# Kernel optimization log

Measured on AMD Instinct MI355X. Metric: run time of the kernel, lower is better.

Reference implementation:

```python
import jax, jax.numpy as jnp
from jax import lax
import numpy as np

DN = ('NCDHW', 'OIDHW', 'NCDHW')
ACTIVE_THRESH = 1


def setup_inputs() -> dict:
    key = jax.random.key(0)
    ks = jax.random.split(key, 10)
    B, D = 4, 64
    chans = [3, 64, 128, 256, 512]
    inp = {
        'x': jax.random.normal(ks[0], (B, 3, D, D, D), jnp.float32),
        'mask': jax.random.randint(ks[1], (B, D, D, D), 0, 20, jnp.int32),
    }
    for i in range(4):
        cin, cout = chans[i], chans[i + 1]
        fan_in = cin * 27
        scale = 1.0 / np.sqrt(fan_in)
        inp[f'w{i+1}'] = jax.random.normal(ks[2 + 2 * i], (cout, cin, 3, 3, 3), jnp.float32) * scale
        inp[f'b{i+1}'] = jax.random.normal(ks[3 + 2 * i], (cout,), jnp.float32) * scale
    return inp


def _sparse_block(x, m, w, b, stride):
    # SparseConv3d(k=3, pad=1) + SparseReLU: output active where 3^3 footprint hits an active input;
    # bias + relu applied only at active sites, inactive sites stay exactly 0 (spconv .dense() semantics).
    s = (stride,) * 3
    pad = [(1, 1)] * 3
    y = lax.conv_general_dilated(x, w, s, pad, dimension_numbers=DN)
    ones = jnp.ones((1, 1, 3, 3, 3), x.dtype)
    m_out = lax.conv_general_dilated(m[:, None].astype(x.dtype), ones, s, pad, dimension_numbers=DN) > 0
    y = jnp.where(m_out, jax.nn.relu(y + b[None, :, None, None, None]), jnp.zeros((), x.dtype))
    return y, m_out[:, 0]


def reference(x, mask, w1, b1, w2, b2, w3, b3, w4, b4):
    m = mask < ACTIVE_THRESH                       # [B,D,H,W] active voxels
    h = x * m[:, None].astype(x.dtype)             # zero inactive input features
    h, m = _sparse_block(h, m, w1, b1, 1)          # [B,64,64,64,64]
    h, m = _sparse_block(h, m, w2, b2, 2)          # [B,128,32,32,32]
    h, m = _sparse_block(h, m, w3, b3, 2)          # [B,256,16,16,16]
    h, m = _sparse_block(h, m, w4, b4, 2)          # [B,512,8,8,8]
    pooled = jnp.max(h, axis=(2, 3, 4))            # dense() + amax over D,H,W -> [B,512]
    return jax.nn.leaky_relu(pooled, negative_slope=0.2)
```

## Files before the change

### kernel.cpp

```cpp
#include <hip/hip_runtime.h>

typedef _Float16 f16;
typedef _Float16 half4 __attribute__((ext_vector_type(4)));
typedef _Float16 half8 __attribute__((ext_vector_type(8)));
typedef float f32x4 __attribute__((ext_vector_type(4)));

#define BATCH 4

__device__ __forceinline__ void gload16(const void* g, void* l) {
  __builtin_amdgcn_global_load_lds((const __attribute__((address_space(1))) unsigned int*)g,
                                   (__attribute__((address_space(3))) unsigned int*)l, 16, 0, 0);
}

template<int DP, int ROWB>
__global__ __launch_bounds__(256) void zborder_k(char* __restrict__ buf) {
  int v = blockIdx.x * 256 + threadIdx.x;
  int b = blockIdx.y;
  if (v >= DP * DP * DP) return;
  int w = v % DP; int t = v / DP; int h = t % DP; int d = t / DP;
  bool border = (w == 0) | (w == DP - 1) | (h == 0) | (h == DP - 1) | (d == 0) | (d == DP - 1);
  if (!border) return;
  char* p = buf + ((size_t)b * DP * DP * DP + v) * ROWB;
  #pragma unroll
  for (int i = 0; i < ROWB; i += 8)
    *reinterpret_cast<unsigned long long*>(p + i) = 0ull;
}

__global__ __launch_bounds__(256) void wprep_k(const float* __restrict__ w,
                                               f16* __restrict__ w27, int COUT, int CIN) {
  int idx = blockIdx.x * 256 + threadIdx.x;
  int total = COUT * CIN * 27;
  if (idx >= total) return;
  int k = idx % 27;
  int t = idx / 27;
  int ci = t % CIN;
  int co = t / CIN;
  w27[((size_t)k * COUT + co) * CIN + ci] = (f16)w[idx];
}

__global__ __launch_bounds__(256) void wprep1_k(const float* __restrict__ w,
                                                f16* __restrict__ wf) {
  int idx = blockIdx.x * 256 + threadIdx.x;
  if (idx >= 64 * 128) return;
  int q = idx & 127, co = idx >> 7;
  int k = q >> 2, ci = q & 3;
  float v = (ci < 3 && k < 27) ? w[(co * 3 + ci) * 27 + k] : 0.f;
  wf[idx] = (f16)v;
}

__global__ __launch_bounds__(256) void xmask_k(const float* __restrict__ x,
                                               const int* __restrict__ mask,
                                               f16* __restrict__ xcp) {
  const int D3 = 262144, PD = 66, PD3 = PD * PD * PD;
  int v = blockIdx.x * 256 + threadIdx.x;
  int b = blockIdx.y;
  bool act = mask[(size_t)b * D3 + v] < 1;
  const float* xb = x + (size_t)b * 3 * D3 + v;
  half4 o;
  o[0] = act ? (f16)xb[0] : (f16)0.f;
  o[1] = act ? (f16)xb[D3] : (f16)0.f;
  o[2] = act ? (f16)xb[2 * D3] : (f16)0.f;
  o[3] = (f16)0.f;
  int ow = v & 63, oh = (v >> 6) & 63, od = v >> 12;
  size_t pv = ((size_t)(od + 1) * PD + oh + 1) * PD + ow + 1;
  *reinterpret_cast<half4*>(xcp + ((size_t)b * PD3 + pv) * 4) = o;
}

__global__ __launch_bounds__(256) void dil_w_k(const int* __restrict__ mask,
                                               unsigned char* __restrict__ aw) {
  const int D3 = 262144;
  int t = blockIdx.x * 256 + threadIdx.x;
  int b = t >> 16;
  int v = (t & 65535) * 4;
  int w0 = v & 63;
  const int* mb = mask + (size_t)b * D3;
  int a[6];
  a[0] = (w0 > 0) ? (mb[v - 1] < 1) : 0;
  #pragma unroll
  for (int i = 0; i < 4; i++) a[i + 1] = mb[v + i] < 1;
  a[5] = (w0 < 60) ? (mb[v + 4] < 1) : 0;
  unsigned int o = 0;
  #pragma unroll
  for (int i = 0; i < 4; i++)
    o |= ((unsigned)(a[i] | a[i + 1] | a[i + 2])) << (8 * i);
  *reinterpret_cast<unsigned int*>(aw + (size_t)b * D3 + v) = o;
}

template<int STRIDE, int DIMSHIFT>
__global__ __launch_bounds__(256) void dil_hd_k(const unsigned char* __restrict__ ai,
                                                unsigned char* __restrict__ ao) {
  const int D3 = 262144;
  int t = blockIdx.x * 256 + threadIdx.x;
  int b = t >> 16;
  int v = (t & 65535) * 4;
  int c = (v >> DIMSHIFT) & 63;
  const unsigned char* ib = ai + (size_t)b * D3;
  unsigned int m = *reinterpret_cast<const unsigned int*>(ib + v);
  if (c > 0)  m |= *reinterpret_cast<const unsigned int*>(ib + v - STRIDE);
  if (c < 63) m |= *reinterpret_cast<const unsigned int*>(ib + v + STRIDE);
  *reinterpret_cast<unsigned int*>(ao + (size_t)b * D3 + v) = m;
}

template<int DIN, int DOUT>
__global__ __launch_bounds__(256) void dilate_s2_k(const unsigned char* __restrict__ mi,
                                                   unsigned char* __restrict__ mo) {
  const int Do3 = DOUT * DOUT * DOUT;
  int v = blockIdx.x * 256 + threadIdx.x;
  if (v >= Do3) return;
  int b = blockIdx.y;
  int ow = v % DOUT, t = v / DOUT, oh = t % DOUT, od = t / DOUT;
  const unsigned char* ib = mi + (size_t)b * DIN * DIN * DIN;
  int act = 0;
  for (int kd = 0; kd < 3; kd++) { int id = od * 2 - 1 + kd; if ((unsigned)id >= (unsigned)DIN) continue;
    for (int kh = 0; kh < 3; kh++) { int ih = oh * 2 - 1 + kh; if ((unsigned)ih >= (unsigned)DIN) continue;
      for (int kw = 0; kw < 3; kw++) { int iw = ow * 2 - 1 + kw; if ((unsigned)iw >= (unsigned)DIN) continue;
        act |= ib[((size_t)id * DIN + ih) * DIN + iw];
      } } }
  mo[(size_t)b * Do3 + v] = (unsigned char)(act ? 1 : 0);
}

template<int BM>
__global__ __launch_bounds__(256) void conv1_mfma_k(const f16* __restrict__ xcp,
                                                    const f16* __restrict__ w1f,
                                                    const float* __restrict__ bias,
                                                    const unsigned char* __restrict__ mo,
                                                    f16* __restrict__ out ) {
  const int D3 = 262144, COUT = 64, PD = 66, PD3 = PD * PD * PD;
  constexpr int K = 128, LD = K + 8;
  constexpr int WM = 2, WN = 2;
  constexpr int MF = BM / (16 * WM), NF = 64 / (16 * WN);
  __shared__ __align__(16) f16 As[BM][LD];
  __shared__ __align__(16) f16 Bs[64][LD];

  const int tid = threadIdx.x, lane = tid & 63, wave = tid >> 6;
  const int wm = wave >> 1, wn = wave & 1;
  const int v0 = blockIdx.x * BM;
  const int b = blockIdx.y;
  const f16* xb = xcp + (size_t)b * PD3 * 4;

  for (int c = tid; c < 64 * (K / 8); c += 256) {
    int row = c >> 4, cc = c & 15;
    *reinterpret_cast<half8*>(&Bs[row][cc * 8]) =
        *reinterpret_cast<const half8*>(w1f + row * K + cc * 8);
  }
  {
    const int row = tid & (BM - 1);
    const int v = v0 + row;
    const int ow = v & 63, oh = (v >> 6) & 63, od = v >> 12;
    const int base = (od * PD + oh) * PD + ow;
    for (int e = tid; e < 32 * BM; e += 256) {
      int kslot = e / BM;
      half4 val = {};
      if (kslot < 27) {
        int kd = kslot / 9, r2 = kslot - kd * 9, kh = r2 / 3, kw = r2 - kh * 3;
        val = *reinterpret_cast<const half4*>(xb + (size_t)(base + (kd * PD + kh) * PD + kw) * 4);
      }
      *reinterpret_cast<half4*>(&As[row][kslot * 4]) = val;
    }
  }
  __syncthreads();

  f32x4 acc[MF][NF] = {};
  const int chanoff = (lane >> 4) << 3;
  const int arow = wm * MF * 16 + (lane & 15);
  const int brow = wn * NF * 16 + (lane & 15);
  #pragma unroll
  for (int q0 = 0; q0 < K; q0 += 32) {
    half8 a[MF], bb[NF];
    #pragma unroll
    for (int mf = 0; mf < MF; mf++)
      a[mf] = *reinterpret_cast<const half8*>(&As[arow + mf * 16][q0 + chanoff]);
    #pragma unroll
    for (int nf = 0; nf < NF; nf++)
      bb[nf] = *reinterpret_cast<const half8*>(&Bs[brow + nf * 16][q0 + chanoff]);
    #pragma unroll
    for (int mf = 0; mf < MF; mf++)
      #pragma unroll
      for (int nf = 0; nf < NF; nf++)
        acc[mf][nf] = __builtin_amdgcn_mfma_f32_16x16x32_f16(a[mf], bb[nf], acc[mf][nf], 0, 0, 0);
  }

  const unsigned char* mb = mo + (size_t)b * D3;
  f16* ob = out + (size_t)b * PD3 * COUT;
  const int ll = lane & 15, lh = lane >> 4;
  float bv[NF];
  #pragma unroll
  for (int nf = 0; nf < NF; nf++) bv[nf] = bias[wn * NF * 16 + nf * 16 + ll];
  #pragma unroll
  for (int mf = 0; mf < MF; mf++) {
    #pragma unroll
    for (int r = 0; r < 4; r++) {
      int v = v0 + wm * MF * 16 + mf * 16 + (lh << 2) + r;
      bool act = mb[v] != 0;
      int ow = v & 63, oh = (v >> 6) & 63, od = v >> 12;
      size_t pv = ((size_t)(od + 1) * PD + oh + 1) * PD + ow + 1;
      #pragma unroll
      for (int nf = 0; nf < NF; nf++) {
        int co = wn * NF * 16 + nf * 16 + ll;
        float val = acc[mf][nf][r] + bv[nf];
        val = act ? (val > 0.f ? val : 0.f) : 0.f;
        ob[pv * COUT + co] = (f16)val;
      }
    }
  }
}

template<int CINS, int CINF, int COUT, int DIN, int DOUT, int BM, int BN,
         int WM, int WN, int SWZ, int OP>
__global__ __launch_bounds__(WM * WN * 64) void conv_mfma2_k(const f16* __restrict__ in,
                                                             const f16* __restrict__ w27,
                                                             const float* __restrict__ bias,
                                                             const unsigned char* __restrict__ mo,
                                                             f16* __restrict__ out) {
  constexpr int PD = DIN + 2, PDo = DOUT + 2;
  constexpr int NW = WM * WN;
  constexpr int MF = BM / (16 * WM), NF = BN / (16 * WN);
  constexpr int ROWB = CINS * 2;
  constexpr int ROWBF = CINF * 2;
  constexpr int CHUNKS = ROWB / 16;
  constexpr int RPI = 64 / CHUNKS;
  constexpr int A_IW = BM / RPI / NW;
  constexpr int B_IW = BN / RPI / NW;
  constexpr int CIH = CINF / CINS;
  constexpr int NSTEP = 27 * CIH;
  constexpr int D3o = DOUT * DOUT * DOUT;
  constexpr int LOGD = (DOUT == 32) ? 5 : ((DOUT == 16) ? 4 : 3);

  __shared__ __align__(16) char As[2][BM * ROWB];
  __shared__ __align__(16) char Bs[2][BN * ROWB];

  const int tid = threadIdx.x, lane = tid & 63, wave = tid >> 6;
  const int wm = wave / WN, wn = wave % WN;
  int bx = blockIdx.x;
  if (SWZ) {
    int cpx = gridDim.x >> 3;
    bx = (bx & 7) * cpx + (bx >> 3);
  }
  const int v0 = bx * BM, co0 = blockIdx.y * BN, b = blockIdx.z;
  const char* ib = (const char*)(in + (size_t)b * PD * PD * PD * CINF);

  const int lrow = lane / CHUNKS;
  const int lchunk = lane % CHUNKS;
  const char* a_src[A_IW];
  #pragma unroll
  for (int i = 0; i < A_IW; i++) {
    int r = (wave * A_IW + i) * RPI + lrow;
    int v = v0 + r;
    int ow = v & (DOUT - 1), oh = (v >> LOGD) & (DOUT - 1), od = v >> (2 * LOGD);
    size_t flat = ((size_t)(2 * od) * PD + 2 * oh) * PD + 2 * ow;
    a_src[i] = ib + flat * ROWBF + (lchunk ^ (r & 7)) * 16;
  }
  const char* b_src[B_IW];
  #pragma unroll
  for (int i = 0; i < B_IW; i++) {
    int r = (wave * B_IW + i) * RPI + lrow;
    b_src[i] = (const char*)w27 + (size_t)(co0 + r) * ROWBF + (lchunk ^ (r & 7)) * 16;
  }

  auto stage = [&](int buf, int s) {
    int k = (CIH == 2) ? (s >> 1) : s;
    int h = (CIH == 2) ? (s & 1) : 0;
    int kd = k / 9, r2 = k - kd * 9, kh = r2 / 3, kw = r2 - kh * 3;
    int koff = ((kd * PD + kh) * PD + kw) * ROWBF + h * ROWB;
    #pragma unroll
    for (int i = 0; i < A_IW; i++)
      gload16(a_src[i] + koff, &As[buf][(wave * A_IW + i) * 1024]);
    size_t wko = (size_t)k * COUT * ROWBF + h * ROWB;
    #pragma unroll
    for (int i = 0; i < B_IW; i++)
      gload16(b_src[i] + wko, &Bs[buf][(wave * B_IW + i) * 1024]);
  };

  f32x4 acc[MF][NF] = {};
  const int ll = lane & 15, lh = lane >> 4;
  const int ra0 = wm * MF * 16 + ll;
  const int rb0 = wn * NF * 16 + ll;
  const int rswa = ra0 & 7;
  const int rswb = rb0 & 7;

  stage(0, 0);
  __syncthreads();
  int cur = 0;
  for (int s = 0; s < NSTEP; s++) {
    if (s < NSTEP - 1) stage(cur ^ 1, s + 1);
    #pragma unroll
    for (int ci0 = 0; ci0 < CINS; ci0 += 32) {
      const int q = (ci0 >> 3) + lh;
      half8 a[MF], bb[NF];
      #pragma unroll
      for (int mf = 0; mf < MF; mf++)
        a[mf] = *reinterpret_cast<const half8*>(
            &As[cur][(ra0 + mf * 16) * ROWB + ((q ^ rswa) * 16)]);
      #pragma unroll
      for (int nf = 0; nf < NF; nf++)
        bb[nf] = *reinterpret_cast<const half8*>(
            &Bs[cur][(rb0 + nf * 16) * ROWB + ((q ^ rswb) * 16)]);
      #pragma unroll
      for (int mf = 0; mf < MF; mf++)
        #pragma unroll
        for (int nf = 0; nf < NF; nf++)
          acc[mf][nf] = __builtin_amdgcn_mfma_f32_16x16x32_f16(a[mf], bb[nf], acc[mf][nf], 0, 0, 0);
    }
    __syncthreads();
    cur ^= 1;
  }

  const unsigned char* mb = mo + (size_t)b * D3o;
  f16* ob = out + (size_t)b * (OP ? PDo * PDo * PDo : D3o) * COUT;
  float bv[NF];
  #pragma unroll
  for (int nf = 0; nf < NF; nf++) bv[nf] = bias[co0 + wn * NF * 16 + nf * 16 + ll];
  #pragma unroll
  for (int mf = 0; mf < MF; mf++) {
    #pragma unroll
    for (int r = 0; r < 4; r++) {
      int v = v0 + wm * MF * 16 + mf * 16 + (lh << 2) + r;
      bool act = mb[v] != 0;
      int ow = v & (DOUT - 1), oh = (v >> LOGD) & (DOUT - 1), od = v >> (2 * LOGD);
      size_t pv = OP ? (((size_t)(od + 1) * PDo + oh + 1) * PDo + ow + 1) : (size_t)v;
      #pragma unroll
      for (int nf = 0; nf < NF; nf++) {
        int co = co0 + wn * NF * 16 + nf * 16 + ll;
        float val = acc[mf][nf][r] + bv[nf];
        val = act ? (val > 0.f ? val : 0.f) : 0.f;
        ob[pv * COUT + co] = (f16)val;
      }
    }
  }
}

__global__ __launch_bounds__(256) void pool_k(const f16* __restrict__ h4,
                                              float* __restrict__ outp) {
  __shared__ float red[4][64];
  int b = blockIdx.y;
  int cl = threadIdx.x & 63;
  int co = blockIdx.x * 64 + cl;
  int vg = threadIdx.x >> 6;
  const f16* p = h4 + (size_t)b * 512 * 512;
  float m = 0.f;
  for (int v = vg * 128; v < vg * 128 + 128; v++) m = fmaxf(m, (float)p[(size_t)v * 512 + co]);
  red[vg][cl] = m;
  __syncthreads();
  if (threadIdx.x < 64) {
    m = fmaxf(fmaxf(red[0][threadIdx.x], red[1][threadIdx.x]),
              fmaxf(red[2][threadIdx.x], red[3][threadIdx.x]));
    float r = (m >= 0.f) ? m : 0.2f * m;
    outp[b * 512 + blockIdx.x * 64 + threadIdx.x] = r;
  }
}

extern "C" void kernel_launch(void* const* d_in, const int* in_sizes, int n_in,
                              void* d_out, int out_size, void* d_ws, size_t ws_size,
                              hipStream_t stream) {
  const float* x    = (const float*)d_in[0];
  const int*   mask = (const int*)d_in[1];
  const float* w1 = (const float*)d_in[2];
  const float* b1 = (const float*)d_in[3];
  const float* w2 = (const float*)d_in[4];
  const float* b2 = (const float*)d_in[5];
  const float* w3 = (const float*)d_in[6];
  const float* b3 = (const float*)d_in[7];
  const float* w4 = (const float*)d_in[8];
  const float* b4 = (const float*)d_in[9];
  float* outp = (float*)d_out;

  const size_t PD1 = 66 * 66 * 66;
  const size_t PD2 = 34 * 34 * 34;
  const size_t PD3s = 18 * 18 * 18;

  char* ws = (char*)d_ws;
  size_t off = 0;
  auto alloc = [&](size_t bytes) -> char* {
    char* p = ws + off;
    off = (off + bytes + 255) & ~(size_t)255;
    return p;
  };
  f16* wf1 = (f16*)alloc((size_t)64 * 128 * 2);
  f16* wf2 = (f16*)alloc((size_t)27 * 128 * 64 * 2);
  f16* wf3 = (f16*)alloc((size_t)27 * 256 * 128 * 2);
  f16* wf4 = (f16*)alloc((size_t)27 * 512 * 256 * 2);
  unsigned char* aw = (unsigned char*)alloc((size_t)BATCH * 262144);
  unsigned char* ah = (unsigned char*)alloc((size_t)BATCH * 262144);
  unsigned char* m1 = (unsigned char*)alloc((size_t)BATCH * 262144);
  unsigned char* m2 = (unsigned char*)alloc((size_t)BATCH * 32768);
  unsigned char* m3 = (unsigned char*)alloc((size_t)BATCH * 4096);
  unsigned char* m4 = (unsigned char*)alloc((size_t)BATCH * 512);
  f16* h1p = (f16*)alloc((size_t)BATCH * PD1 * 64 * 2);
  f16* h2p = (f16*)alloc((size_t)BATCH * PD2 * 128 * 2);
  f16* h3p = (f16*)alloc((size_t)BATCH * PD3s * 256 * 2);
  f16* h4  = (f16*)alloc((size_t)BATCH * 512 * 512 * 2);
  f16* xcp = h3p;
  if (off > ws_size) return;

  wprep1_k<<<dim3((64 * 128 + 255) / 256), 256, 0, stream>>>(w1, wf1);
  wprep_k<<<dim3((128 * 64 * 27 + 255) / 256), 256, 0, stream>>>(w2, wf2, 128, 64);
  wprep_k<<<dim3((256 * 128 * 27 + 255) / 256), 256, 0, stream>>>(w3, wf3, 256, 128);
  wprep_k<<<dim3((512 * 256 * 27 + 255) / 256), 256, 0, stream>>>(w4, wf4, 512, 256);

  dil_w_k<<<dim3(BATCH * 65536 / 256), 256, 0, stream>>>(mask, aw);
  dil_hd_k<64, 6><<<dim3(BATCH * 65536 / 256), 256, 0, stream>>>(aw, ah);
  dil_hd_k<4096, 12><<<dim3(BATCH * 65536 / 256), 256, 0, stream>>>(ah, m1);
  dilate_s2_k<64, 32><<<dim3(128, BATCH), 256, 0, stream>>>(m1, m2);
  dilate_s2_k<32, 16><<<dim3(16, BATCH), 256, 0, stream>>>(m2, m3);
  dilate_s2_k<16, 8><<<dim3(2, BATCH), 256, 0, stream>>>(m3, m4);

  xmask_k<<<dim3(1024, BATCH), 256, 0, stream>>>(x, mask, xcp);
  zborder_k<66, 8><<<dim3((287496 + 255) / 256, BATCH), 256, 0, stream>>>((char*)xcp);
  zborder_k<66, 128><<<dim3((287496 + 255) / 256, BATCH), 256, 0, stream>>>((char*)h1p);
  zborder_k<34, 256><<<dim3((39304 + 255) / 256, BATCH), 256, 0, stream>>>((char*)h2p);

  conv1_mfma_k<128><<<dim3(262144 / 128, BATCH), 256, 0, stream>>>(xcp, wf1, b1, m1, h1p);

  zborder_k<18, 512><<<dim3((5832 + 255) / 256, BATCH), 256, 0, stream>>>((char*)h3p);

  conv_mfma2_k<64, 64, 128, 64, 32, 64, 128, 2, 2, 1, 1>
      <<<dim3(512, 1, BATCH), 256, 0, stream>>>(h1p, wf2, b2, m2, h2p);
  conv_mfma2_k<64, 128, 256, 32, 16, 64, 64, 2, 2, 0, 1>
      <<<dim3(64, 4, BATCH), 256, 0, stream>>>(h2p, wf3, b3, m3, h3p);
  conv_mfma2_k<128, 256, 512, 16, 8, 32, 64, 1, 2, 0, 0>
      <<<dim3(16, 8, BATCH), 128, 0, stream>>>(h3p, wf4, b4, m4, h4);

  pool_k<<<dim3(8, BATCH), 256, 0, stream>>>(h4, outp);
}
```

Measured before the change: 351.8 us.

## Load conv weights directly into registers, enlarge tiles, merge batch in conv4

The implicit-GEMM conv kernel stops staging weight tiles in shared memory. Each lane now loads its B fragments straight from global memory into registers, double-buffered across step pairs, while only the activation tile still goes through LDS. Tile sizes grow (BM 128 for conv2, BN 128 for conv3, 64x128 with 4 waves for conv4), and conv4 folds the batch into the M dimension to get larger tiles and fewer blocks. This cuts LDS traffic and footprint but adds register pressure and uncoalesced global weight reads that rely on cache reuse.

```diff
diff --git a/kernel.cpp b/kernel.cpp
--- a/kernel.cpp
+++ b/kernel.cpp
@@ -206,8 +206,8 @@
 }
 
 template<int CINS, int CINF, int COUT, int DIN, int DOUT, int BM, int BN,
-         int WM, int WN, int SWZ, int OP>
-__global__ __launch_bounds__(WM * WN * 64) void conv_mfma2_k(const f16* __restrict__ in,
+         int WM, int WN, int SWZ, int OP, int BMERGE>
+__global__ __launch_bounds__(WM * WN * 64) void conv_mfmaR_k(const f16* __restrict__ in,
                                                              const f16* __restrict__ w27,
                                                              const float* __restrict__ bias,
                                                              const unsigned char* __restrict__ mo,
@@ -220,14 +220,14 @@
   constexpr int CHUNKS = ROWB / 16;
   constexpr int RPI = 64 / CHUNKS;
   constexpr int A_IW = BM / RPI / NW;
-  constexpr int B_IW = BN / RPI / NW;
   constexpr int CIH = CINF / CINS;
   constexpr int NSTEP = 27 * CIH;
+  constexpr int CI0S = CINS / 32;
+  constexpr int NBF = NF * CI0S;
   constexpr int D3o = DOUT * DOUT * DOUT;
   constexpr int LOGD = (DOUT == 32) ? 5 : ((DOUT == 16) ? 4 : 3);
 
   __shared__ __align__(16) char As[2][BM * ROWB];
-  __shared__ __align__(16) char Bs[2][BN * ROWB];
 
   const int tid = threadIdx.x, lane = tid & 63, wave = tid >> 6;
   const int wm = wave / WN, wn = wave % WN;
@@ -236,8 +236,8 @@
     int cpx = gridDim.x >> 3;
     bx = (bx & 7) * cpx + (bx >> 3);
   }
-  const int v0 = bx * BM, co0 = blockIdx.y * BN, b = blockIdx.z;
-  const char* ib = (const char*)(in + (size_t)b * PD * PD * PD * CINF);
+  const int v0 = bx * BM, co0 = blockIdx.y * BN;
+  const int bz = BMERGE ? 0 : blockIdx.z;
 
   const int lrow = lane / CHUNKS;
   const int lchunk = lane % CHUNKS;
@@ -246,18 +246,21 @@
   for (int i = 0; i < A_IW; i++) {
     int r = (wave * A_IW + i) * RPI + lrow;
     int v = v0 + r;
-    int ow = v & (DOUT - 1), oh = (v >> LOGD) & (DOUT - 1), od = v >> (2 * LOGD);
-    size_t flat = ((size_t)(2 * od) * PD + 2 * oh) * PD + 2 * ow;
-    a_src[i] = ib + flat * ROWBF + (lchunk ^ (r & 7)) * 16;
-  }
-  const char* b_src[B_IW];
-  #pragma unroll
-  for (int i = 0; i < B_IW; i++) {
-    int r = (wave * B_IW + i) * RPI + lrow;
-    b_src[i] = (const char*)w27 + (size_t)(co0 + r) * ROWBF + (lchunk ^ (r & 7)) * 16;
-  }
-
-  auto stage = [&](int buf, int s) {
+    int vb = BMERGE ? (v >> (3 * LOGD)) : bz;
+    int vv = BMERGE ? (v & (D3o - 1)) : v;
+    int ow = vv & (DOUT - 1), oh = (vv >> LOGD) & (DOUT - 1), od = vv >> (2 * LOGD);
+    size_t flat = (size_t)vb * PD * PD * PD + ((size_t)(2 * od) * PD + 2 * oh) * PD + 2 * ow;
+    a_src[i] = (const char*)in + flat * ROWBF + (lchunk ^ (r & 7)) * 16;
+  }
+  const int ll = lane & 15, lh = lane >> 4;
+  const char* b_src[NF];
+  #pragma unroll
+  for (int nf = 0; nf < NF; nf++) {
+    int row = co0 + wn * NF * 16 + nf * 16 + ll;
+    b_src[nf] = (const char*)w27 + (size_t)row * ROWBF + lh * 16;
+  }
+
+  auto stageA = [&](int buf, int s) {
     int k = (CIH == 2) ? (s >> 1) : s;
     int h = (CIH == 2) ? (s & 1) : 0;
     int kd = k / 9, r2 = k - kd * 9, kh = r2 / 3, kw = r2 - kh * 3;
@@ -265,48 +268,59 @@
     #pragma unroll
     for (int i = 0; i < A_IW; i++)
       gload16(a_src[i] + koff, &As[buf][(wave * A_IW + i) * 1024]);
+  };
+
+  auto loadB = [&](half8 (&br)[NBF], int s) {
+    int k = (CIH == 2) ? (s >> 1) : s;
+    int h = (CIH == 2) ? (s & 1) : 0;
     size_t wko = (size_t)k * COUT * ROWBF + h * ROWB;
     #pragma unroll
-    for (int i = 0; i < B_IW; i++)
-      gload16(b_src[i] + wko, &Bs[buf][(wave * B_IW + i) * 1024]);
+    for (int nf = 0; nf < NF; nf++)
+      #pragma unroll
+      for (int c = 0; c < CI0S; c++)
+        br[nf * CI0S + c] = *reinterpret_cast<const half8*>(b_src[nf] + wko + c * 64);
   };
 
   f32x4 acc[MF][NF] = {};
-  const int ll = lane & 15, lh = lane >> 4;
   const int ra0 = wm * MF * 16 + ll;
-  const int rb0 = wn * NF * 16 + ll;
   const int rswa = ra0 & 7;
-  const int rswb = rb0 & 7;
-
-  stage(0, 0);
-  __syncthreads();
-  int cur = 0;
-  for (int s = 0; s < NSTEP; s++) {
-    if (s < NSTEP - 1) stage(cur ^ 1, s + 1);
-    #pragma unroll
-    for (int ci0 = 0; ci0 < CINS; ci0 += 32) {
-      const int q = (ci0 >> 3) + lh;
-      half8 a[MF], bb[NF];
+
+  auto compute = [&](const char* Ab, half8 (&br)[NBF]) {
+    #pragma unroll
+    for (int c = 0; c < CI0S; c++) {
+      const int q = c * 4 + lh;
+      half8 a[MF];
       #pragma unroll
       for (int mf = 0; mf < MF; mf++)
         a[mf] = *reinterpret_cast<const half8*>(
-            &As[cur][(ra0 + mf * 16) * ROWB + ((q ^ rswa) * 16)]);
-      #pragma unroll
-      for (int nf = 0; nf < NF; nf++)
-        bb[nf] = *reinterpret_cast<const half8*>(
-            &Bs[cur][(rb0 + nf * 16) * ROWB + ((q ^ rswb) * 16)]);
+            &Ab[(ra0 + mf * 16) * ROWB + ((q ^ rswa) * 16)]);
       #pragma unroll
       for (int mf = 0; mf < MF; mf++)
         #pragma unroll
         for (int nf = 0; nf < NF; nf++)
-          acc[mf][nf] = __builtin_amdgcn_mfma_f32_16x16x32_f16(a[mf], bb[nf], acc[mf][nf], 0, 0, 0);
+          acc[mf][nf] = __builtin_amdgcn_mfma_f32_16x16x32_f16(a[mf], br[nf * CI0S + c],
+                                                               acc[mf][nf], 0, 0, 0);
     }
+  };
+
+  half8 bA[NBF], bB[NBF];
+  stageA(0, 0);
+  loadB(bA, 0);
+  __syncthreads();
+  constexpr int NPAIR = NSTEP / 2;
+  for (int sp = 0; sp < NPAIR; sp++) {
+    int s1 = 2 * sp + 1;
+    stageA(1, s1);
+    loadB(bB, s1);
+    compute(As[0], bA);
     __syncthreads();
-    cur ^= 1;
-  }
-
-  const unsigned char* mb = mo + (size_t)b * D3o;
-  f16* ob = out + (size_t)b * (OP ? PDo * PDo * PDo : D3o) * COUT;
+    if (s1 + 1 < NSTEP) { stageA(0, s1 + 1); loadB(bA, s1 + 1); }
+    compute(As[1], bB);
+    __syncthreads();
+  }
+  if (NSTEP & 1) compute(As[0], bA);
+
+  f16* ob = out;
   float bv[NF];
   #pragma unroll
   for (int nf = 0; nf < NF; nf++) bv[nf] = bias[co0 + wn * NF * 16 + nf * 16 + ll];
@@ -315,15 +329,18 @@
     #pragma unroll
     for (int r = 0; r < 4; r++) {
       int v = v0 + wm * MF * 16 + mf * 16 + (lh << 2) + r;
-      bool act = mb[v] != 0;
-      int ow = v & (DOUT - 1), oh = (v >> LOGD) & (DOUT - 1), od = v >> (2 * LOGD);
-      size_t pv = OP ? (((size_t)(od + 1) * PDo + oh + 1) * PDo + ow + 1) : (size_t)v;
+      int vb = BMERGE ? (v >> (3 * LOGD)) : bz;
+      int vv = BMERGE ? (v & (D3o - 1)) : v;
+      bool act = mo[(size_t)vb * D3o + vv] != 0;
+      int ow = vv & (DOUT - 1), oh = (vv >> LOGD) & (DOUT - 1), od = vv >> (2 * LOGD);
+      size_t pv = OP ? (((size_t)(od + 1) * PDo + oh + 1) * PDo + ow + 1) : (size_t)vv;
+      size_t obase = ((size_t)vb * (OP ? PDo * PDo * PDo : D3o) + pv) * COUT;
       #pragma unroll
       for (int nf = 0; nf < NF; nf++) {
         int co = co0 + wn * NF * 16 + nf * 16 + ll;
         float val = acc[mf][nf][r] + bv[nf];
         val = act ? (val > 0.f ? val : 0.f) : 0.f;
-        ob[pv * COUT + co] = (f16)val;
+        ob[obase + co] = (f16)val;
       }
     }
   }
@@ -413,12 +430,12 @@
 
   zborder_k<18, 512><<<dim3((5832 + 255) / 256, BATCH), 256, 0, stream>>>((char*)h3p);
 
-  conv_mfma2_k<64, 64, 128, 64, 32, 64, 128, 2, 2, 1, 1>
-      <<<dim3(512, 1, BATCH), 256, 0, stream>>>(h1p, wf2, b2, m2, h2p);
-  conv_mfma2_k<64, 128, 256, 32, 16, 64, 64, 2, 2, 0, 1>
-      <<<dim3(64, 4, BATCH), 256, 0, stream>>>(h2p, wf3, b3, m3, h3p);
-  conv_mfma2_k<128, 256, 512, 16, 8, 32, 64, 1, 2, 0, 0>
-      <<<dim3(16, 8, BATCH), 128, 0, stream>>>(h3p, wf4, b4, m4, h4);
+  conv_mfmaR_k<64, 64, 128, 64, 32, 128, 128, 2, 2, 1, 1, 0>
+      <<<dim3(256, 1, BATCH), 256, 0, stream>>>(h1p, wf2, b2, m2, h2p);
+  conv_mfmaR_k<64, 128, 256, 32, 16, 64, 128, 2, 2, 1, 1, 0>
+      <<<dim3(64, 2, BATCH), 256, 0, stream>>>(h2p, wf3, b3, m3, h3p);
+  conv_mfmaR_k<128, 256, 512, 16, 8, 64, 128, 2, 2, 0, 0, 1>
+      <<<dim3(32, 4, 1), 256, 0, stream>>>(h3p, wf4, b4, m4, h4);
 
   pool_k<<<dim3(8, BATCH), 256, 0, stream>>>(h4, outp);
 }
```

Result: slower. 513.1 us (+45.8%).

## Retile strided conv kernels, merge batch into M dimension, narrow K slices

Applied to the files above, without the earlier changes.

Adds a BMERGE mode that folds the batch index into the voxel (M) dimension, so conv3/conv4 launch larger tiles over a flattened batch-voxel space. K slices shrink to 32 or 64 channels, with a generalized swizzle key for fewer chunks per row. Block tiles grow to 128x128 for conv2/conv3 and conv4 uses 1x4 waves with BN=128, with swizzled block order enabled. The intent is more operand reuse per block and better occupancy balance on the small later layers, at the cost of more pipeline steps and synchronizations per block.

```diff
diff --git a/kernel.cpp b/kernel.cpp
--- a/kernel.cpp
+++ b/kernel.cpp
@@ -206,7 +206,7 @@
 }
 
 template<int CINS, int CINF, int COUT, int DIN, int DOUT, int BM, int BN,
-         int WM, int WN, int SWZ, int OP>
+         int WM, int WN, int SWZ, int OP, int BMERGE>
 __global__ __launch_bounds__(WM * WN * 64) void conv_mfma2_k(const f16* __restrict__ in,
                                                              const f16* __restrict__ w27,
                                                              const float* __restrict__ bias,
@@ -223,6 +223,7 @@
   constexpr int B_IW = BN / RPI / NW;
   constexpr int CIH = CINF / CINS;
   constexpr int NSTEP = 27 * CIH;
+  constexpr int CI0S = CINS / 32;
   constexpr int D3o = DOUT * DOUT * DOUT;
   constexpr int LOGD = (DOUT == 32) ? 5 : ((DOUT == 16) ? 4 : 3);
 
@@ -236,8 +237,10 @@
     int cpx = gridDim.x >> 3;
     bx = (bx & 7) * cpx + (bx >> 3);
   }
-  const int v0 = bx * BM, co0 = blockIdx.y * BN, b = blockIdx.z;
-  const char* ib = (const char*)(in + (size_t)b * PD * PD * PD * CINF);
+  const int v0 = bx * BM, co0 = blockIdx.y * BN;
+  const int bz = BMERGE ? 0 : blockIdx.z;
+
+  auto key = [](int r) -> int { return (CHUNKS >= 8) ? (r & 7) : ((r >> 1) & 3); };
 
   const int lrow = lane / CHUNKS;
   const int lchunk = lane % CHUNKS;
@@ -246,20 +249,22 @@
   for (int i = 0; i < A_IW; i++) {
     int r = (wave * A_IW + i) * RPI + lrow;
     int v = v0 + r;
-    int ow = v & (DOUT - 1), oh = (v >> LOGD) & (DOUT - 1), od = v >> (2 * LOGD);
-    size_t flat = ((size_t)(2 * od) * PD + 2 * oh) * PD + 2 * ow;
-    a_src[i] = ib + flat * ROWBF + (lchunk ^ (r & 7)) * 16;
+    int vb = BMERGE ? (v >> (3 * LOGD)) : bz;
+    int vv = BMERGE ? (v & (D3o - 1)) : v;
+    int ow = vv & (DOUT - 1), oh = (vv >> LOGD) & (DOUT - 1), od = vv >> (2 * LOGD);
+    size_t flat = (size_t)vb * PD * PD * PD + ((size_t)(2 * od) * PD + 2 * oh) * PD + 2 * ow;
+    a_src[i] = (const char*)in + flat * ROWBF + (lchunk ^ key(r)) * 16;
   }
   const char* b_src[B_IW];
   #pragma unroll
   for (int i = 0; i < B_IW; i++) {
     int r = (wave * B_IW + i) * RPI + lrow;
-    b_src[i] = (const char*)w27 + (size_t)(co0 + r) * ROWBF + (lchunk ^ (r & 7)) * 16;
+    b_src[i] = (const char*)w27 + (size_t)(co0 + r) * ROWBF + (lchunk ^ key(r)) * 16;
   }
 
   auto stage = [&](int buf, int s) {
-    int k = (CIH == 2) ? (s >> 1) : s;
-    int h = (CIH == 2) ? (s & 1) : 0;
+    int k = s / CIH;
+    int h = s - k * CIH;
     int kd = k / 9, r2 = k - kd * 9, kh = r2 / 3, kw = r2 - kh * 3;
     int koff = ((kd * PD + kh) * PD + kw) * ROWBF + h * ROWB;
     #pragma unroll
@@ -275,8 +280,8 @@
   const int ll = lane & 15, lh = lane >> 4;
   const int ra0 = wm * MF * 16 + ll;
   const int rb0 = wn * NF * 16 + ll;
-  const int rswa = ra0 & 7;
-  const int rswb = rb0 & 7;
+  const int rswa = key(ra0);
+  const int rswb = key(rb0);
 
   stage(0, 0);
   __syncthreads();
@@ -284,8 +289,8 @@
   for (int s = 0; s < NSTEP; s++) {
     if (s < NSTEP - 1) stage(cur ^ 1, s + 1);
     #pragma unroll
-    for (int ci0 = 0; ci0 < CINS; ci0 += 32) {
-      const int q = (ci0 >> 3) + lh;
+    for (int c = 0; c < CI0S; c++) {
+      const int q = c * 4 + lh;
       half8 a[MF], bb[NF];
       #pragma unroll
       for (int mf = 0; mf < MF; mf++)
@@ -305,8 +310,7 @@
     cur ^= 1;
   }
 
-  const unsigned char* mb = mo + (size_t)b * D3o;
-  f16* ob = out + (size_t)b * (OP ? PDo * PDo * PDo : D3o) * COUT;
+  f16* ob = out;
   float bv[NF];
   #pragma unroll
   for (int nf = 0; nf < NF; nf++) bv[nf] = bias[co0 + wn * NF * 16 + nf * 16 + ll];
@@ -315,15 +319,18 @@
     #pragma unroll
     for (int r = 0; r < 4; r++) {
       int v = v0 + wm * MF * 16 + mf * 16 + (lh << 2) + r;
-      bool act = mb[v] != 0;
-      int ow = v & (DOUT - 1), oh = (v >> LOGD) & (DOUT - 1), od = v >> (2 * LOGD);
-      size_t pv = OP ? (((size_t)(od + 1) * PDo + oh + 1) * PDo + ow + 1) : (size_t)v;
+      int vb = BMERGE ? (v >> (3 * LOGD)) : bz;
+      int vv = BMERGE ? (v & (D3o - 1)) : v;
+      bool act = mo[(size_t)vb * D3o + vv] != 0;
+      int ow = vv & (DOUT - 1), oh = (vv >> LOGD) & (DOUT - 1), od = vv >> (2 * LOGD);
+      size_t pv = OP ? (((size_t)(od + 1) * PDo + oh + 1) * PDo + ow + 1) : (size_t)vv;
+      size_t obase = ((size_t)vb * (OP ? PDo * PDo * PDo : D3o) + pv) * COUT;
       #pragma unroll
       for (int nf = 0; nf < NF; nf++) {
         int co = co0 + wn * NF * 16 + nf * 16 + ll;
         float val = acc[mf][nf][r] + bv[nf];
         val = act ? (val > 0.f ? val : 0.f) : 0.f;
-        ob[pv * COUT + co] = (f16)val;
+        ob[obase + co] = (f16)val;
       }
     }
   }
@@ -413,12 +420,12 @@
 
   zborder_k<18, 512><<<dim3((5832 + 255) / 256, BATCH), 256, 0, stream>>>((char*)h3p);
 
-  conv_mfma2_k<64, 64, 128, 64, 32, 64, 128, 2, 2, 1, 1>
-      <<<dim3(512, 1, BATCH), 256, 0, stream>>>(h1p, wf2, b2, m2, h2p);
-  conv_mfma2_k<64, 128, 256, 32, 16, 64, 64, 2, 2, 0, 1>
-      <<<dim3(64, 4, BATCH), 256, 0, stream>>>(h2p, wf3, b3, m3, h3p);
-  conv_mfma2_k<128, 256, 512, 16, 8, 32, 64, 1, 2, 0, 0>
-      <<<dim3(16, 8, BATCH), 128, 0, stream>>>(h3p, wf4, b4, m4, h4);
+  conv_mfma2_k<32, 64, 128, 64, 32, 128, 128, 2, 2, 1, 1, 0>
+      <<<dim3(256, 1, BATCH), 256, 0, stream>>>(h1p, wf2, b2, m2, h2p);
+  conv_mfma2_k<32, 128, 256, 32, 16, 128, 128, 2, 2, 1, 1, 1>
+      <<<dim3(128, 2, 1), 256, 0, stream>>>(h2p, wf3, b3, m3, h3p);
+  conv_mfma2_k<64, 256, 512, 16, 8, 32, 128, 1, 4, 1, 0, 1>
+      <<<dim3(64, 4, 1), 256, 0, stream>>>(h3p, wf4, b4, m4, h4);
 
   pool_k<<<dim3(8, BATCH), 256, 0, stream>>>(h4, outp);
 }
```

Result: slower. 437.9 us (+24.4%).
